# Kernel tuning notes

Measured on AMD Instinct MI355X. Metric: run time of the kernel, lower is better.

Reference implementation:

```python
import jax, jax.numpy as jnp
import numpy as np

B, H, W, ENC = 32, 14, 14, 2048
T = 21            # sequence length; 20 decode steps
V, E, A, L = 10000, 512, 512, 512
P = H * W


def setup_inputs() -> dict:
    key = jax.random.key(0)
    ks = jax.random.split(key, 24)
    g = lambda k, shape, s=0.02: (jax.random.normal(k, shape, jnp.float32) * s)
    return {
        "encoder_output": jax.random.normal(ks[0], (B, H, W, ENC), jnp.float32),
        # tokens in [1, V) so sign/abs length count gives full-length sequences
        "sequences": jax.random.randint(ks[1], (B, T), 1, V).astype(jnp.int64),
        "emb": g(ks[2], (V, E)),
        "Wea": g(ks[3], (ENC, A)), "bea": jnp.zeros((A,), jnp.float32),
        "Wga": g(ks[4], (L, A)),   "bga": jnp.zeros((A,), jnp.float32),
        "Wfa": g(ks[5], (A, 1)),   "bfa": jnp.zeros((1,), jnp.float32),
        "Wl": g(ks[6], (E + ENC, 4 * L)), "Ul": g(ks[7], (L, 4 * L)),
        "bl": jnp.zeros((4 * L,), jnp.float32),
        "Wim": g(ks[8], (ENC, L)), "bim": jnp.zeros((L,), jnp.float32),
        "Wic": g(ks[9], (ENC, L)), "bic": jnp.zeros((L,), jnp.float32),
        "Wb": g(ks[10], (L, ENC)), "bb": jnp.zeros((ENC,), jnp.float32),
        "Wo": g(ks[11], (L, V)),   "bo": jnp.zeros((V,), jnp.float32),
    }


def reference(encoder_output, sequences, emb, Wea, bea, Wga, bga, Wfa, bfa,
              Wl, Ul, bl, Wim, bim, Wic, bic, Wb, bb, Wo, bo):
    # --- sort by descending length (packed-sequence style) ---
    lengths = jnp.sum(jnp.sign(jnp.abs(sequences)), axis=1).astype(jnp.int32)
    order = jnp.argsort(-lengths)
    lengths = lengths[order] - 1                       # number of decode steps per row
    enc = encoder_output[order].reshape(B, P, ENC)     # [B, P, ENC]
    seqs = sequences[order]

    # --- init LSTM states from mean-pooled encoder features ---
    mean = enc.mean(axis=1)                            # [B, ENC]
    h0 = mean @ Wim + bim                              # 'memory_state' (plays role of h)
    c0 = mean @ Wic + bic                              # 'carry_state'  (plays role of c)

    # encoder side of additive attention is time-invariant: hoist out of the loop
    a1 = enc @ Wea + bea                               # [B, P, A]

    steps = T - 1
    toks = seqs[:, :steps].T                           # [steps, B] teacher-forced inputs
    masks = lengths[None, :] > jnp.arange(steps)[:, None]  # [steps, B] active rows

    def step(carry, xs):
        h, c = carry
        tok, m = xs
        # additive attention on carry (cell) state, as in the original code
        a2 = c @ Wga + bga                                         # [B, A]
        e = jnp.squeeze(jax.nn.relu(a1 + a2[:, None, :]) @ Wfa + bfa, -1)  # [B, P]
        alpha = jax.nn.softmax(e, axis=1)
        awe = jnp.einsum('bpe,bp->be', enc, alpha)                 # [B, ENC]
        beta = jax.nn.sigmoid(c @ Wb + bb)                         # gating
        x = jnp.concatenate([emb[tok], awe * beta], axis=1)        # [B, E+ENC]
        # Keras LSTMCell: gate order i, f, g, o
        z = x @ Wl + h @ Ul + bl
        zi, zf, zg, zo = jnp.split(z, 4, axis=1)
        c_new = jax.nn.sigmoid(zf) * c + jax.nn.sigmoid(zi) * jnp.tanh(zg)
        h_new = jax.nn.sigmoid(zo) * jnp.tanh(c_new)
        mf = m[:, None].astype(h.dtype)
        h_new = h_new * mf                 # zero-pad finished rows (packed semantics)
        c_new = c_new * mf
        pred = (c_new @ Wo + bo) * mf      # prediction from carry (cell) state, dropout off
        return (h_new, c_new), (pred, alpha * mf)

    (_, _), (preds, alphas) = jax.lax.scan(step, (h0, c0), (toks, masks))
    return preds.transpose(1, 0, 2), alphas.transpose(1, 0, 2), order
```

## Files before the change

### kernel.cpp

```cpp
#include <hip/hip_runtime.h>
#include <math.h>

#define B_    32
#define T_    21
#define STEPS 20
#define V_    10000
#define E_    512
#define A_    512
#define L_    512
#define P_    196
#define ENC_  2048
#define XW_   3072
#define NT2_  792
#define N2_   12672

#define WS_ORD    0
#define WS_SLEN   32
#define WS_CBUF   64
#define WS_CB     32832
#define WS_XB     41024
#define WS_A2S    90176
#define WS_ESH    106560
#define WS_BETA   114752
#define WS_PZ4    180288
#define WS_A1B    442432
#define WS_WZP    2048064
#define WS_WCP    5193792
#define WS_MEAN   8437824
#define WS_PH     8503360
#define WS_WEAT   9027648

#define OUT_PRED  0
#define OUT_ALPHA 6400000
#define OUT_ORDER 6525440

typedef __attribute__((ext_vector_type(8))) short bf16x8;
typedef __attribute__((ext_vector_type(4))) float f32x4;
typedef unsigned short ushort_t;

__device__ inline unsigned f2bf2(float lo, float hi) {
    unsigned a = __float_as_uint(lo), b = __float_as_uint(hi);
    a = (a + 0x7FFFu + ((a >> 16) & 1u)) >> 16;
    b = (b + 0x7FFFu + ((b >> 16) & 1u)) >> 16;
    return a | (b << 16);
}
__device__ inline ushort_t f2bf(float f) {
    unsigned u = __float_as_uint(f);
    return (ushort_t)((u + 0x7FFFu + ((u >> 16) & 1u)) >> 16);
}
__device__ inline float bfu_lo(unsigned u) { return __uint_as_float(u << 16); }
__device__ inline float bfu_hi(unsigned u) { return __uint_as_float(u & 0xFFFF0000u); }

__global__ void k_order(const int* __restrict__ seqs, int* __restrict__ ord,
                        int* __restrict__ slen, float* __restrict__ out_ord)
{
    __shared__ int len[B_];
    int i = threadIdx.x;
    if (i < B_) {
        int c = 0;
        for (int t = 0; t < T_; ++t) c += (seqs[i * T_ + t] != 0) ? 1 : 0;
        len[i] = c;
    }
    __syncthreads();
    if (i < B_) {
        int li = len[i], r = 0;
        for (int j = 0; j < B_; ++j) {
            int lj = len[j];
            if (lj > li || (lj == li && j < i)) ++r;
        }
        ord[r] = i; slen[r] = li - 1; out_ord[r] = (float)i;
    }
}

__global__ void k_mean(const float* __restrict__ enc, const int* __restrict__ ord,
                       float* __restrict__ mean)
{
    int tid = blockIdx.x * 256 + threadIdx.x;
    int b = tid >> 11, e = tid & 2047;
    const float* row = enc + (size_t)ord[b] * (P_ * ENC_) + e;
    float s = 0.f;
    for (int p = 0; p < P_; ++p) s += row[(size_t)p * ENC_];
    mean[tid] = s * (1.0f / 196.0f);
}

__global__ void k_castWT(const float* __restrict__ Wea, ushort_t* __restrict__ WT)
{
    int tid = blockIdx.x * 256 + threadIdx.x;
    int n = tid >> 11, k = tid & 2047;
    WT[tid] = f2bf(Wea[(size_t)k * 512 + n]);
}

__global__ void sg_partial(const float* __restrict__ X, const float* __restrict__ W,
                           float* __restrict__ part, int K, int N, int kchunk, int chunk_ofs)
{
    const int n = blockIdx.x * 256 + threadIdx.x;
    const int c = blockIdx.y;
    const int bh = blockIdx.z;
    const int k0 = c * kchunk;
    int k1 = k0 + kchunk; if (k1 > K) k1 = K;
    float acc[16];
#pragma unroll
    for (int b = 0; b < 16; ++b) acc[b] = 0.f;
    if (n < N) {
        const float* Xb = X + (size_t)(bh * 16) * K;
        for (int k = k0; k < k1; k += 4) {
            float w0 = W[(size_t)(k + 0) * N + n];
            float w1 = W[(size_t)(k + 1) * N + n];
            float w2 = W[(size_t)(k + 2) * N + n];
            float w3 = W[(size_t)(k + 3) * N + n];
#pragma unroll
            for (int b = 0; b < 16; ++b) {
                const float4 xv = *reinterpret_cast<const float4*>(&Xb[(size_t)b * K + k]);
                acc[b] += xv.x * w0 + xv.y * w1 + xv.z * w2 + xv.w * w3;
            }
        }
        float* po = part + (size_t)(chunk_ofs + c) * (B_ * (size_t)N) + (size_t)(bh * 16) * N;
#pragma unroll
        for (int b = 0; b < 16; ++b) po[(size_t)b * N + n] = acc[b];
    }
}

__global__ void k_h0c0(const float* __restrict__ ph, const float* __restrict__ bim,
                       const float* __restrict__ bic, float* __restrict__ c0,
                       ushort_t* __restrict__ cB, ushort_t* __restrict__ XB)
{
    int tid = blockIdx.x * 256 + threadIdx.x;
    int half = tid >> 14;
    int idx = tid & 16383;
    int l = idx & 511, b = idx >> 9;
    int cofs = half ? 16 : 0;
    float s = 0.f;
    for (int c = 0; c < 16; ++c) s += ph[(size_t)(cofs + c) * (B_ * 512) + idx];
    if (half) {
        float cv = s + bic[l];
        c0[idx] = cv;
        cB[idx] = f2bf(cv);
    } else {
        XB[(size_t)b * XW_ + 2560 + l] = f2bf(s + bim[l]);
    }
}

__global__ __launch_bounds__(256, 1) void k_a1_mfma(
    const float* __restrict__ enc, const ushort_t* __restrict__ WeaT,
    const float* __restrict__ bea, const int* __restrict__ ord,
    ushort_t* __restrict__ a1b)
{
    __shared__ ushort_t As[2][128 * 40];
    __shared__ ushort_t Bs[2][128 * 40];
    const int tid = threadIdx.x;
    const int lane = tid & 63, wave = tid >> 6;
    const int m0 = blockIdx.x * 128;
    const int n0 = blockIdx.y * 128;

    const int c0 = tid, c1 = tid + 256;
    const int ar0 = c0 >> 2, ak0 = (c0 & 3) * 8;
    const int ar1 = c1 >> 2, ak1 = (c1 & 3) * 8;
    const int g0 = m0 + ar0, g1 = m0 + ar1;
    const float* Ag0 = enc + ((size_t)ord[g0 / P_] * P_ + (g0 % P_)) * ENC_ + ak0;
    const float* Ag1 = enc + ((size_t)ord[g1 / P_] * P_ + (g1 % P_)) * ENC_ + ak1;
    const ushort_t* Bg0 = WeaT + (size_t)(n0 + ar0) * ENC_ + ak0;
    const ushort_t* Bg1 = WeaT + (size_t)(n0 + ar1) * ENC_ + ak1;
    const int ao0 = ar0 * 40 + ak0, ao1 = ar1 * 40 + ak1;

    const int wm = (wave >> 1) * 64, wn = (wave & 1) * 64;
    f32x4 acc[4][4] = {};

    {
        float4 v0 = *reinterpret_cast<const float4*>(Ag0);
        float4 v1 = *reinterpret_cast<const float4*>(Ag0 + 4);
        float4 v2 = *reinterpret_cast<const float4*>(Ag1);
        float4 v3 = *reinterpret_cast<const float4*>(Ag1 + 4);
        uint4 pa0, pa1;
        pa0.x = f2bf2(v0.x, v0.y); pa0.y = f2bf2(v0.z, v0.w);
        pa0.z = f2bf2(v1.x, v1.y); pa0.w = f2bf2(v1.z, v1.w);
        pa1.x = f2bf2(v2.x, v2.y); pa1.y = f2bf2(v2.z, v2.w);
        pa1.z = f2bf2(v3.x, v3.y); pa1.w = f2bf2(v3.z, v3.w);
        *reinterpret_cast<uint4*>(&As[0][ao0]) = pa0;
        *reinterpret_cast<uint4*>(&As[0][ao1]) = pa1;
        *reinterpret_cast<uint4*>(&Bs[0][ao0]) = *reinterpret_cast<const uint4*>(Bg0);
        *reinterpret_cast<uint4*>(&Bs[0][ao1]) = *reinterpret_cast<const uint4*>(Bg1);
    }
    __syncthreads();

    for (int it = 0; it < 64; ++it) {
        const int cur = it & 1;
        uint4 npa0, npa1, npb0, npb1;
        const bool more = (it < 63);
        if (more) {
            const int k0 = (it + 1) * 32;
            float4 v0 = *reinterpret_cast<const float4*>(Ag0 + k0);
            float4 v1 = *reinterpret_cast<const float4*>(Ag0 + k0 + 4);
            float4 v2 = *reinterpret_cast<const float4*>(Ag1 + k0);
            float4 v3 = *reinterpret_cast<const float4*>(Ag1 + k0 + 4);
            npa0.x = f2bf2(v0.x, v0.y); npa0.y = f2bf2(v0.z, v0.w);
            npa0.z = f2bf2(v1.x, v1.y); npa0.w = f2bf2(v1.z, v1.w);
            npa1.x = f2bf2(v2.x, v2.y); npa1.y = f2bf2(v2.z, v2.w);
            npa1.z = f2bf2(v3.x, v3.y); npa1.w = f2bf2(v3.z, v3.w);
            npb0 = *reinterpret_cast<const uint4*>(Bg0 + k0);
            npb1 = *reinterpret_cast<const uint4*>(Bg1 + k0);
        }
        {
            bf16x8 af[4], bfr[4];
            const int arow = wm + (lane & 15);
            const int brow = wn + (lane & 15);
            const int koff = (lane >> 4) * 8;
#pragma unroll
            for (int mt = 0; mt < 4; ++mt)
                af[mt] = *reinterpret_cast<const bf16x8*>(&As[cur][(arow + mt * 16) * 40 + koff]);
#pragma unroll
            for (int nt = 0; nt < 4; ++nt)
                bfr[nt] = *reinterpret_cast<const bf16x8*>(&Bs[cur][(brow + nt * 16) * 40 + koff]);
#pragma unroll
            for (int mt = 0; mt < 4; ++mt)
#pragma unroll
                for (int nt = 0; nt < 4; ++nt)
                    acc[mt][nt] = __builtin_amdgcn_mfma_f32_16x16x32_bf16(
                        af[mt], bfr[nt], acc[mt][nt], 0, 0, 0);
        }
        if (more) {
            const int nxt = cur ^ 1;
            *reinterpret_cast<uint4*>(&As[nxt][ao0]) = npa0;
            *reinterpret_cast<uint4*>(&As[nxt][ao1]) = npa1;
            *reinterpret_cast<uint4*>(&Bs[nxt][ao0]) = npb0;
            *reinterpret_cast<uint4*>(&Bs[nxt][ao1]) = npb1;
        }
        __syncthreads();
    }
    const int rbase = (lane >> 4) * 4;
    const int cbase = lane & 15;
#pragma unroll
    for (int nt = 0; nt < 4; ++nt) {
        int col = n0 + wn + nt * 16 + cbase;
        float be = bea[col];
#pragma unroll
        for (int mt = 0; mt < 4; ++mt) {
            int row = m0 + wm + mt * 16 + rbase;
#pragma unroll
            for (int r = 0; r < 4; ++r)
                a1b[(size_t)(row + r) * 512 + col] = f2bf(acc[mt][nt][r] + be);
        }
    }
}

__global__ void k_packWz(const float* __restrict__ Wl, const float* __restrict__ Ul,
                         ushort_t* __restrict__ Wz)
{
    const unsigned tidg = blockIdx.x * 256 + threadIdx.x;
    const int l = tidg & 63;
    const unsigned rem = tidg >> 6;
    const int kt = rem % 96;
    const int nt = rem / 96;
    const int k = kt * 32 + ((l >> 4) << 3);
    const int n = nt * 16 + (l & 15);
    float v[8];
#pragma unroll
    for (int j = 0; j < 8; ++j) {
        int kr = k + j;
        v[j] = (kr < 2560) ? Wl[(size_t)kr * 2048 + n] : Ul[(size_t)(kr - 2560) * 2048 + n];
    }
    uint4 o;
    o.x = f2bf2(v[0], v[1]); o.y = f2bf2(v[2], v[3]);
    o.z = f2bf2(v[4], v[5]); o.w = f2bf2(v[6], v[7]);
    *reinterpret_cast<uint4*>(Wz + (size_t)tidg * 8) = o;
}

__global__ void k_packWc(const float* __restrict__ Wb, const float* __restrict__ Wga,
                         const float* __restrict__ Wo, ushort_t* __restrict__ Wc)
{
    const unsigned tidg = blockIdx.x * 256 + threadIdx.x;
    const int l = tidg & 63;
    const int kt = (tidg >> 6) & 15;
    const int nt = tidg >> 10;
    const int k = kt * 32 + ((l >> 4) << 3);
    const int n = nt * 16 + (l & 15);
    float v[8];
#pragma unroll
    for (int j = 0; j < 8; ++j) {
        int kr = k + j;
        float x;
        if (n < 2048)            x = Wb[(size_t)kr * 2048 + n];
        else if (n < 2560)       x = Wga[(size_t)kr * 512 + (n - 2048)];
        else if (n < 2560 + V_)  x = Wo[(size_t)kr * V_ + (n - 2560)];
        else                     x = 0.f;
        v[j] = x;
    }
    uint4 o;
    o.x = f2bf2(v[0], v[1]); o.y = f2bf2(v[2], v[3]);
    o.z = f2bf2(v[4], v[5]); o.w = f2bf2(v[6], v[7]);
    *reinterpret_cast<uint4*>(Wc + (size_t)tidg * 8) = o;
}

__global__ __launch_bounds__(256, 1) void k_e(
    const float* __restrict__ a2s, const float* __restrict__ Wfa,
    const float* __restrict__ bfa, const ushort_t* __restrict__ a1b,
    float* __restrict__ eshW)
{
    __shared__ float a2sh[512];
    __shared__ float wfsh[512];
    const int b = blockIdx.x >> 2, pc = blockIdx.x & 3;
    const int tid = threadIdx.x;
    const int wave = tid >> 6, lane = tid & 63;
    a2sh[tid] = a2s[b * 512 + tid];       a2sh[tid + 256] = a2s[b * 512 + 256 + tid];
    wfsh[tid] = Wfa[tid];                 wfsh[tid + 256] = Wfa[256 + tid];
    __syncthreads();

    const int grp = lane >> 4, sub = lane & 15;
    float4 a2r[4][2], wfr[4][2];
#pragma unroll
    for (int blk = 0; blk < 4; ++blk)
#pragma unroll
        for (int j = 0; j < 2; ++j) {
            int d = blk * 128 + sub * 8 + j * 4;
            a2r[blk][j] = *reinterpret_cast<const float4*>(&a2sh[d]);
            wfr[blk][j] = *reinterpret_cast<const float4*>(&wfsh[d]);
        }
    const float bf0 = bfa[0];
    const int p0 = pc * 49;
#pragma unroll
    for (int pass = 0; pass < 4; ++pass) {
        const int pl = pass * 16 + wave * 4 + grp;
        const bool valid = pl < 49;
        const int p = p0 + (valid ? pl : 0);
        const ushort_t* arow = a1b + ((size_t)b * P_ + p) * 512;
        float s = 0.f;
#pragma unroll
        for (int blk = 0; blk < 4; ++blk) {
            uint4 raw = *reinterpret_cast<const uint4*>(arow + blk * 128 + sub * 8);
            float4 av = a2r[blk][0], wv = wfr[blk][0];
            float v;
            v = bfu_lo(raw.x) + av.x; v = v > 0.f ? v : 0.f; s += v * wv.x;
            v = bfu_hi(raw.x) + av.y; v = v > 0.f ? v : 0.f; s += v * wv.y;
            v = bfu_lo(raw.y) + av.z; v = v > 0.f ? v : 0.f; s += v * wv.z;
            v = bfu_hi(raw.y) + av.w; v = v > 0.f ? v : 0.f; s += v * wv.w;
            av = a2r[blk][1]; wv = wfr[blk][1];
            v = bfu_lo(raw.z) + av.x; v = v > 0.f ? v : 0.f; s += v * wv.x;
            v = bfu_hi(raw.z) + av.y; v = v > 0.f ? v : 0.f; s += v * wv.y;
            v = bfu_lo(raw.w) + av.z; v = v > 0.f ? v : 0.f; s += v * wv.z;
            v = bfu_hi(raw.w) + av.w; v = v > 0.f ? v : 0.f; s += v * wv.w;
        }
        s += __shfl_xor(s, 1, 64);
        s += __shfl_xor(s, 2, 64);
        s += __shfl_xor(s, 4, 64);
        s += __shfl_xor(s, 8, 64);
        if (sub == 0 && valid) eshW[b * 256 + p0 + pl] = s + bf0;
    }
}

__global__ __launch_bounds__(256, 1) void k_awex(
    const float* __restrict__ eshW, const float* __restrict__ enc,
    const int* __restrict__ ord, const int* __restrict__ slen, int t,
    const float* __restrict__ beta, float* __restrict__ out_alpha,
    ushort_t* __restrict__ XB)
{
    __shared__ float red[256];
    __shared__ float alsh[P_];
    const int b = blockIdx.x >> 2, ec = blockIdx.x & 3;
    const int tid = threadIdx.x;

    float v = (tid < P_) ? eshW[b * 256 + tid] : -1e30f;
    red[tid] = v; __syncthreads();
    for (int s2 = 128; s2 > 0; s2 >>= 1) {
        if (tid < s2) red[tid] = fmaxf(red[tid], red[tid + s2]);
        __syncthreads();
    }
    float mx = red[0]; __syncthreads();
    float ex = (tid < P_) ? expf(v - mx) : 0.f;
    red[tid] = ex; __syncthreads();
    for (int s2 = 128; s2 > 0; s2 >>= 1) {
        if (tid < s2) red[tid] += red[tid + s2];
        __syncthreads();
    }
    float inv = 1.0f / red[0];
    float al = ex * inv;
    if (tid < P_) alsh[tid] = al;
    if (ec == 0 && tid < P_) {
        float mf = (slen[b] > t) ? 1.f : 0.f;
        out_alpha[((size_t)b * STEPS + t) * P_ + tid] = al * mf;
    }
    __syncthreads();

    const int e0 = ec * 512 + tid * 2;
    const float* ep = enc + (size_t)ord[b] * (P_ * ENC_) + e0;
    float s0 = 0.f, s1 = 0.f;
    for (int p = 0; p < P_; ++p) {
        float2 u = *reinterpret_cast<const float2*>(ep + (size_t)p * ENC_);
        float ap = alsh[p];
        s0 += ap * u.x; s1 += ap * u.y;
    }
    float2 bt = *reinterpret_cast<const float2*>(&beta[b * 2048 + e0]);
    unsigned pk = f2bf2(s0 * bt.x, s1 * bt.y);
    *reinterpret_cast<unsigned*>(XB + (size_t)b * XW_ + 512 + e0) = pk;
}

__global__ __launch_bounds__(256) void k_zmfma(const ushort_t* __restrict__ XB,
                                               const ushort_t* __restrict__ WzP,
                                               float* __restrict__ pz4)
{
    const int tid = threadIdx.x, lane = tid & 63, w = tid >> 6;
    const int nt = blockIdx.x * 4 + w;
    const int kt0 = blockIdx.y * 24;
    const int ar = lane & 15, ak = (lane >> 4) * 8;
    const ushort_t* A0 = XB + (size_t)ar * XW_ + kt0 * 32 + ak;
    const ushort_t* Bp = WzP + ((size_t)nt * 96 + kt0) * 512 + lane * 8;
    f32x4 acc0 = {}, acc1 = {};
    for (int kt = 0; kt < 24; ++kt) {
        bf16x8 a0 = *reinterpret_cast<const bf16x8*>(A0 + kt * 32);
        bf16x8 a1 = *reinterpret_cast<const bf16x8*>(A0 + 16 * XW_ + kt * 32);
        bf16x8 bf = *reinterpret_cast<const bf16x8*>(Bp + kt * 512);
        acc0 = __builtin_amdgcn_mfma_f32_16x16x32_bf16(a0, bf, acc0, 0, 0, 0);
        acc1 = __builtin_amdgcn_mfma_f32_16x16x32_bf16(a1, bf, acc1, 0, 0, 0);
    }
    const int col = nt * 16 + (lane & 15);
    const int r0 = (lane >> 4) * 4;
    float* po = pz4 + (size_t)blockIdx.y * 65536 + col;
#pragma unroll
    for (int r = 0; r < 4; ++r) {
        po[(size_t)(r0 + r) * 2048] = acc0[r];
        po[(size_t)(16 + r0 + r) * 2048] = acc1[r];
    }
}

__global__ void k_gates(const float* __restrict__ pz4, const float* __restrict__ bl,
                        const float* __restrict__ c_in, const int* __restrict__ slen, int t,
                        float* __restrict__ c_out, ushort_t* __restrict__ cB,
                        ushort_t* __restrict__ XB)
{
    int tid = blockIdx.x * 256 + threadIdx.x;
    int b = tid >> 9, l = tid & 511;
    float zi = 0.f, zf = 0.f, zg = 0.f, zo = 0.f;
#pragma unroll
    for (int kc = 0; kc < 4; ++kc) {
        const float* row = pz4 + (size_t)kc * 65536 + b * 2048;
        zi += row[l]; zf += row[512 + l]; zg += row[1024 + l]; zo += row[1536 + l];
    }
    zi += bl[l]; zf += bl[512 + l]; zg += bl[1024 + l]; zo += bl[1536 + l];
    float si = 1.f / (1.f + expf(-zi));
    float sf = 1.f / (1.f + expf(-zf));
    float so = 1.f / (1.f + expf(-zo));
    float g  = tanhf(zg);
    float cn = sf * c_in[tid] + si * g;
    float hn = so * tanhf(cn);
    float mf = (slen[b] > t) ? 1.f : 0.f;
    cn *= mf; hn *= mf;
    c_out[tid] = cn;
    cB[tid] = f2bf(cn);
    XB[(size_t)b * XW_ + 2560 + l] = f2bf(hn);
}

__global__ __launch_bounds__(256) void k_cmfma(
    const ushort_t* __restrict__ cB, const ushort_t* __restrict__ WcP,
    const float* __restrict__ bb, const float* __restrict__ bga, const float* __restrict__ bo,
    const int* __restrict__ slen, int t, int do_pred, int tnext,
    const int* __restrict__ seqs, const float* __restrict__ emb, const int* __restrict__ ord,
    float* __restrict__ beta, float* __restrict__ a2s, float* __restrict__ out_pred,
    ushort_t* __restrict__ XB)
{
    const int bid = blockIdx.x, tid = threadIdx.x;
    if (bid >= 99) {
        const int g = (bid - 99) * 256 + tid;
        const int b = g >> 4, j0 = (g & 15) * 32;
        const int tok = seqs[ord[b] * T_ + tnext];
        const float4* src = reinterpret_cast<const float4*>(emb + (size_t)tok * E_ + j0);
        uint4* dst = reinterpret_cast<uint4*>(XB + (size_t)b * XW_ + j0);
#pragma unroll
        for (int q = 0; q < 4; ++q) {
            float4 v0 = src[2 * q], v1 = src[2 * q + 1];
            uint4 o;
            o.x = f2bf2(v0.x, v0.y); o.y = f2bf2(v0.z, v0.w);
            o.z = f2bf2(v1.x, v1.y); o.w = f2bf2(v1.z, v1.w);
            dst[q] = o;
        }
        return;
    }
    const int lane = tid & 63, w = tid >> 6;
    const int nt0 = bid * 8 + w * 2;
    const int ar = lane & 15, ak = (lane >> 4) * 8;
    const ushort_t* A0 = cB + ar * 512 + ak;
    const ushort_t* Bp = WcP + (size_t)nt0 * 8192 + lane * 8;
    f32x4 acc[2][2] = {};
    for (int kt = 0; kt < 16; ++kt) {
        bf16x8 a0 = *reinterpret_cast<const bf16x8*>(A0 + kt * 32);
        bf16x8 a1 = *reinterpret_cast<const bf16x8*>(A0 + 16 * 512 + kt * 32);
        bf16x8 b0 = *reinterpret_cast<const bf16x8*>(Bp + kt * 512);
        bf16x8 b1 = *reinterpret_cast<const bf16x8*>(Bp + 8192 + kt * 512);
        acc[0][0] = __builtin_amdgcn_mfma_f32_16x16x32_bf16(a0, b0, acc[0][0], 0, 0, 0);
        acc[0][1] = __builtin_amdgcn_mfma_f32_16x16x32_bf16(a0, b1, acc[0][1], 0, 0, 0);
        acc[1][0] = __builtin_amdgcn_mfma_f32_16x16x32_bf16(a1, b0, acc[1][0], 0, 0, 0);
        acc[1][1] = __builtin_amdgcn_mfma_f32_16x16x32_bf16(a1, b1, acc[1][1], 0, 0, 0);
    }
    const int r0 = (lane >> 4) * 4, cb = lane & 15;
#pragma unroll
    for (int nti = 0; nti < 2; ++nti) {
        const int n = (nt0 + nti) * 16 + cb;
#pragma unroll
        for (int mt = 0; mt < 2; ++mt) {
#pragma unroll
            for (int r = 0; r < 4; ++r) {
                const int brow = mt * 16 + r0 + r;
                float v = acc[mt][nti][r];
                if (n < 2048) {
                    beta[brow * 2048 + n] = 1.f / (1.f + expf(-(v + bb[n])));
                } else if (n < 2560) {
                    a2s[brow * 512 + (n - 2048)] = v + bga[n - 2048];
                } else if (n < 2560 + V_) {
                    if (do_pred) {
                        float mf = (slen[brow] > t) ? 1.f : 0.f;
                        out_pred[((size_t)brow * STEPS + t) * V_ + (n - 2560)] =
                            (v + bo[n - 2560]) * mf;
                    }
                }
            }
        }
    }
}

extern "C" void kernel_launch(void* const* d_in, const int* in_sizes, int n_in,
                              void* d_out, int out_size, void* d_ws, size_t ws_size,
                              hipStream_t stream)
{
    const float* enc  = (const float*)d_in[0];
    const int*   seqs = (const int*)  d_in[1];
    const float* emb  = (const float*)d_in[2];
    const float* Wea  = (const float*)d_in[3];
    const float* bea  = (const float*)d_in[4];
    const float* Wga  = (const float*)d_in[5];
    const float* bga  = (const float*)d_in[6];
    const float* Wfa  = (const float*)d_in[7];
    const float* bfa  = (const float*)d_in[8];
    const float* Wl   = (const float*)d_in[9];
    const float* Ul   = (const float*)d_in[10];
    const float* bl   = (const float*)d_in[11];
    const float* Wim  = (const float*)d_in[12];
    const float* bim  = (const float*)d_in[13];
    const float* Wic  = (const float*)d_in[14];
    const float* bic  = (const float*)d_in[15];
    const float* Wb   = (const float*)d_in[16];
    const float* bb   = (const float*)d_in[17];
    const float* Wo   = (const float*)d_in[18];
    const float* bo   = (const float*)d_in[19];

    float* out = (float*)d_out;
    float* ws  = (float*)d_ws;
    int* ord  = (int*)(ws + WS_ORD);
    int* slen = (int*)(ws + WS_SLEN);
    ushort_t* cBu  = (ushort_t*)(ws + WS_CB);
    ushort_t* XB   = (ushort_t*)(ws + WS_XB);
    ushort_t* a1b  = (ushort_t*)(ws + WS_A1B);
    ushort_t* WzP  = (ushort_t*)(ws + WS_WZP);
    ushort_t* WcP  = (ushort_t*)(ws + WS_WCP);
    ushort_t* WeaT = (ushort_t*)(ws + WS_WEAT);
    float* a2s  = ws + WS_A2S;
    float* eshW = ws + WS_ESH;
    float* beta = ws + WS_BETA;
    float* pz4  = ws + WS_PZ4;

    k_order<<<1, 64, 0, stream>>>(seqs, ord, slen, out + OUT_ORDER);
    k_mean<<<256, 256, 0, stream>>>(enc, ord, ws + WS_MEAN);
    sg_partial<<<dim3(2, 16, 2), 256, 0, stream>>>(ws + WS_MEAN, Wim, ws + WS_PH, 2048, 512, 128, 0);
    sg_partial<<<dim3(2, 16, 2), 256, 0, stream>>>(ws + WS_MEAN, Wic, ws + WS_PH, 2048, 512, 128, 16);
    k_h0c0<<<128, 256, 0, stream>>>(ws + WS_PH, bim, bic, ws + WS_CBUF, cBu, XB);
    k_castWT<<<4096, 256, 0, stream>>>(Wea, WeaT);
    k_a1_mfma<<<dim3(49, 4), 256, 0, stream>>>(enc, WeaT, bea, ord, a1b);
    k_packWz<<<3072, 256, 0, stream>>>(Wl, Ul, WzP);
    k_packWc<<<3168, 256, 0, stream>>>(Wb, Wga, Wo, WcP);
    k_cmfma<<<101, 256, 0, stream>>>(cBu, WcP, bb, bga, bo, slen, 0, 0, 0,
                                     seqs, emb, ord, beta, a2s, out + OUT_PRED, XB);

    for (int t = 0; t < STEPS; ++t) {
        float* c_in  = ws + WS_CBUF + (t & 1) * (B_ * L_);
        float* c_out = ws + WS_CBUF + ((t + 1) & 1) * (B_ * L_);

        k_e<<<128, 256, 0, stream>>>(a2s, Wfa, bfa, a1b, eshW);
        k_awex<<<128, 256, 0, stream>>>(eshW, enc, ord, slen, t, beta, out + OUT_ALPHA, XB);
        k_zmfma<<<dim3(32, 4), 256, 0, stream>>>(XB, WzP, pz4);
        k_gates<<<64, 256, 0, stream>>>(pz4, bl, c_in, slen, t, c_out, cBu, XB);
        k_cmfma<<<101, 256, 0, stream>>>(cBu, WcP, bb, bga, bo, slen, t, 1, t + 1,
                                         seqs, emb, ord, beta, a2s, out + OUT_PRED, XB);
    }
}
```

Before: 1.132 ms.

## Batch output projection across all steps and fuse attention score with weighted sum

The vocabulary projection (c @ Wo) is taken out of the recurrent loop. Each step's bf16 cell state is stored into a per-step buffer, and one large MFMA GEMM (640 x 10000 x 512) runs after the loop, so Wo is streamed once instead of twenty times. The per-step kernel now only computes the beta and a2 columns, which shrinks it to 22 blocks. The attention-score kernel and the softmax/weighted-sum kernel are fused into one kernel that keeps scores in shared memory and splits the pixel range across waves. Workspace regions for the setup-only buffers are aliased onto the packed weight areas to make room for the per-step cell states.

```diff
diff --git a/kernel.cpp b/kernel.cpp
--- a/kernel.cpp
+++ b/kernel.cpp
@@ -11,24 +11,22 @@
 #define P_    196
 #define ENC_  2048
 #define XW_   3072
-#define NT2_  792
-#define N2_   12672
 
 #define WS_ORD    0
 #define WS_SLEN   32
 #define WS_CBUF   64
-#define WS_CB     32832
-#define WS_XB     41024
-#define WS_A2S    90176
-#define WS_ESH    106560
-#define WS_BETA   114752
-#define WS_PZ4    180288
-#define WS_A1B    442432
-#define WS_WZP    2048064
-#define WS_WCP    5193792
-#define WS_MEAN   8437824
-#define WS_PH     8503360
-#define WS_WEAT   9027648
+#define WS_CB0    32832
+#define WS_CBALL  36928
+#define WS_XB     200768
+#define WS_A2S    249920
+#define WS_BETA   266304
+#define WS_PZ4    331840
+#define WS_A1B    593984
+#define WS_WZP    2199616
+#define WS_WCP    5345344
+#define WS_MEAN   (WS_WZP)
+#define WS_PH     (WS_WZP + 65536)
+#define WS_WEAT   (WS_WCP)
 
 #define OUT_PRED  0
 #define OUT_ALPHA 6400000
@@ -122,7 +120,7 @@
 
 __global__ void k_h0c0(const float* __restrict__ ph, const float* __restrict__ bim,
                        const float* __restrict__ bic, float* __restrict__ c0,
-                       ushort_t* __restrict__ cB, ushort_t* __restrict__ XB)
+                       ushort_t* __restrict__ cB0, ushort_t* __restrict__ XB)
 {
     int tid = blockIdx.x * 256 + threadIdx.x;
     int half = tid >> 14;
@@ -134,7 +132,7 @@
     if (half) {
         float cv = s + bic[l];
         c0[idx] = cv;
-        cB[idx] = f2bf(cv);
+        cB0[idx] = f2bf(cv);
     } else {
         XB[(size_t)b * XW_ + 2560 + l] = f2bf(s + bim[l]);
     }
@@ -290,14 +288,19 @@
     *reinterpret_cast<uint4*>(Wc + (size_t)tidg * 8) = o;
 }
 
-__global__ __launch_bounds__(256, 1) void k_e(
+__global__ __launch_bounds__(256, 1) void k_eawex(
     const float* __restrict__ a2s, const float* __restrict__ Wfa,
     const float* __restrict__ bfa, const ushort_t* __restrict__ a1b,
-    float* __restrict__ eshW)
+    const float* __restrict__ enc, const int* __restrict__ ord,
+    const int* __restrict__ slen, int t, const float* __restrict__ beta,
+    float* __restrict__ out_alpha, ushort_t* __restrict__ XB)
 {
     __shared__ float a2sh[512];
     __shared__ float wfsh[512];
-    const int b = blockIdx.x >> 2, pc = blockIdx.x & 3;
+    __shared__ float esh[208];
+    __shared__ float red[256];
+    __shared__ float part[4][512];
+    const int b = blockIdx.x >> 2, ec = blockIdx.x & 3;
     const int tid = threadIdx.x;
     const int wave = tid >> 6, lane = tid & 63;
     a2sh[tid] = a2s[b * 512 + tid];       a2sh[tid + 256] = a2s[b * 512 + 256 + tid];
@@ -315,12 +318,11 @@
             wfr[blk][j] = *reinterpret_cast<const float4*>(&wfsh[d]);
         }
     const float bf0 = bfa[0];
-    const int p0 = pc * 49;
-#pragma unroll
-    for (int pass = 0; pass < 4; ++pass) {
+#pragma unroll
+    for (int pass = 0; pass < 13; ++pass) {
         const int pl = pass * 16 + wave * 4 + grp;
-        const bool valid = pl < 49;
-        const int p = p0 + (valid ? pl : 0);
+        const bool valid = pl < P_;
+        const int p = valid ? pl : 0;
         const ushort_t* arow = a1b + ((size_t)b * P_ + p) * 512;
         float s = 0.f;
 #pragma unroll
@@ -342,22 +344,11 @@
         s += __shfl_xor(s, 2, 64);
         s += __shfl_xor(s, 4, 64);
         s += __shfl_xor(s, 8, 64);
-        if (sub == 0 && valid) eshW[b * 256 + p0 + pl] = s + bf0;
-    }
-}
-
-__global__ __launch_bounds__(256, 1) void k_awex(
-    const float* __restrict__ eshW, const float* __restrict__ enc,
-    const int* __restrict__ ord, const int* __restrict__ slen, int t,
-    const float* __restrict__ beta, float* __restrict__ out_alpha,
-    ushort_t* __restrict__ XB)
-{
-    __shared__ float red[256];
-    __shared__ float alsh[P_];
-    const int b = blockIdx.x >> 2, ec = blockIdx.x & 3;
-    const int tid = threadIdx.x;
-
-    float v = (tid < P_) ? eshW[b * 256 + tid] : -1e30f;
+        if (sub == 0 && valid) esh[pl] = s + bf0;
+    }
+    __syncthreads();
+
+    float v = (tid < P_) ? esh[tid] : -1e30f;
     red[tid] = v; __syncthreads();
     for (int s2 = 128; s2 > 0; s2 >>= 1) {
         if (tid < s2) red[tid] = fmaxf(red[tid], red[tid + s2]);
@@ -372,24 +363,34 @@
     }
     float inv = 1.0f / red[0];
     float al = ex * inv;
-    if (tid < P_) alsh[tid] = al;
+    __syncthreads();
+    if (tid < P_) esh[tid] = al;
     if (ec == 0 && tid < P_) {
         float mf = (slen[b] > t) ? 1.f : 0.f;
         out_alpha[((size_t)b * STEPS + t) * P_ + tid] = al * mf;
     }
     __syncthreads();
 
-    const int e0 = ec * 512 + tid * 2;
-    const float* ep = enc + (size_t)ord[b] * (P_ * ENC_) + e0;
-    float s0 = 0.f, s1 = 0.f;
-    for (int p = 0; p < P_; ++p) {
-        float2 u = *reinterpret_cast<const float2*>(ep + (size_t)p * ENC_);
-        float ap = alsh[p];
-        s0 += ap * u.x; s1 += ap * u.y;
-    }
-    float2 bt = *reinterpret_cast<const float2*>(&beta[b * 2048 + e0]);
-    unsigned pk = f2bf2(s0 * bt.x, s1 * bt.y);
-    *reinterpret_cast<unsigned*>(XB + (size_t)b * XW_ + 512 + e0) = pk;
+    const int col0 = ec * 512 + lane * 8;
+    const float* ep = enc + (size_t)ord[b] * (P_ * ENC_) + (size_t)wave * 49 * ENC_ + col0;
+    float s8[8] = {0.f, 0.f, 0.f, 0.f, 0.f, 0.f, 0.f, 0.f};
+    for (int i = 0; i < 49; ++i) {
+        float ap = esh[wave * 49 + i];
+        float4 u0 = *reinterpret_cast<const float4*>(ep + (size_t)i * ENC_);
+        float4 u1 = *reinterpret_cast<const float4*>(ep + (size_t)i * ENC_ + 4);
+        s8[0] += ap * u0.x; s8[1] += ap * u0.y; s8[2] += ap * u0.z; s8[3] += ap * u0.w;
+        s8[4] += ap * u1.x; s8[5] += ap * u1.y; s8[6] += ap * u1.z; s8[7] += ap * u1.w;
+    }
+#pragma unroll
+    for (int j = 0; j < 8; ++j) part[wave][lane * 8 + j] = s8[j];
+    __syncthreads();
+    const int cc = tid * 2;
+    float r0 = part[0][cc] + part[1][cc] + part[2][cc] + part[3][cc];
+    float r1 = part[0][cc + 1] + part[1][cc + 1] + part[2][cc + 1] + part[3][cc + 1];
+    const int col = ec * 512 + cc;
+    float2 bt = *reinterpret_cast<const float2*>(&beta[b * 2048 + col]);
+    unsigned pk = f2bf2(r0 * bt.x, r1 * bt.y);
+    *reinterpret_cast<unsigned*>(XB + (size_t)b * XW_ + 512 + col) = pk;
 }
 
 __global__ __launch_bounds__(256) void k_zmfma(const ushort_t* __restrict__ XB,
@@ -422,7 +423,7 @@
 
 __global__ void k_gates(const float* __restrict__ pz4, const float* __restrict__ bl,
                         const float* __restrict__ c_in, const int* __restrict__ slen, int t,
-                        float* __restrict__ c_out, ushort_t* __restrict__ cB,
+                        float* __restrict__ c_out, ushort_t* __restrict__ cB_slot,
                         ushort_t* __restrict__ XB)
 {
     int tid = blockIdx.x * 256 + threadIdx.x;
@@ -443,21 +444,20 @@
     float mf = (slen[b] > t) ? 1.f : 0.f;
     cn *= mf; hn *= mf;
     c_out[tid] = cn;
-    cB[tid] = f2bf(cn);
+    cB_slot[tid] = f2bf(cn);
     XB[(size_t)b * XW_ + 2560 + l] = f2bf(hn);
 }
 
-__global__ __launch_bounds__(256) void k_cmfma(
+__global__ __launch_bounds__(256) void k_cmfma_lite(
     const ushort_t* __restrict__ cB, const ushort_t* __restrict__ WcP,
-    const float* __restrict__ bb, const float* __restrict__ bga, const float* __restrict__ bo,
-    const int* __restrict__ slen, int t, int do_pred, int tnext,
-    const int* __restrict__ seqs, const float* __restrict__ emb, const int* __restrict__ ord,
-    float* __restrict__ beta, float* __restrict__ a2s, float* __restrict__ out_pred,
-    ushort_t* __restrict__ XB)
+    const float* __restrict__ bb, const float* __restrict__ bga,
+    int tnext, const int* __restrict__ seqs, const float* __restrict__ emb,
+    const int* __restrict__ ord,
+    float* __restrict__ beta, float* __restrict__ a2s, ushort_t* __restrict__ XB)
 {
     const int bid = blockIdx.x, tid = threadIdx.x;
-    if (bid >= 99) {
-        const int g = (bid - 99) * 256 + tid;
+    if (bid >= 20) {
+        const int g = (bid - 20) * 256 + tid;
         const int b = g >> 4, j0 = (g & 15) * 32;
         const int tok = seqs[ord[b] * T_ + tnext];
         const float4* src = reinterpret_cast<const float4*>(emb + (size_t)tok * E_ + j0);
@@ -500,14 +500,58 @@
                 float v = acc[mt][nti][r];
                 if (n < 2048) {
                     beta[brow * 2048 + n] = 1.f / (1.f + expf(-(v + bb[n])));
-                } else if (n < 2560) {
+                } else {
                     a2s[brow * 512 + (n - 2048)] = v + bga[n - 2048];
-                } else if (n < 2560 + V_) {
-                    if (do_pred) {
-                        float mf = (slen[brow] > t) ? 1.f : 0.f;
-                        out_pred[((size_t)brow * STEPS + t) * V_ + (n - 2560)] =
-                            (v + bo[n - 2560]) * mf;
-                    }
+                }
+            }
+        }
+    }
+}
+
+__global__ __launch_bounds__(256) void k_pred(
+    const ushort_t* __restrict__ cBall, const ushort_t* __restrict__ WcP,
+    const float* __restrict__ bo, const int* __restrict__ slen,
+    float* __restrict__ out_pred)
+{
+    const int tid = threadIdx.x, lane = tid & 63, w = tid >> 6;
+    const int n0 = blockIdx.x * 128;
+    const int m0 = blockIdx.y * 128;
+    const int wm = (w >> 1) * 64, wn = (w & 1) * 64;
+    const int ar = lane & 15, ak = (lane >> 4) * 8;
+    const int ntb = (2560 + n0 + wn) >> 4;
+    f32x4 acc[4][4] = {};
+    for (int kt = 0; kt < 16; ++kt) {
+        bf16x8 af[4], bfr[4];
+#pragma unroll
+        for (int mt = 0; mt < 4; ++mt)
+            af[mt] = *reinterpret_cast<const bf16x8*>(
+                cBall + (size_t)(m0 + wm + mt * 16 + ar) * 512 + kt * 32 + ak);
+#pragma unroll
+        for (int nt = 0; nt < 4; ++nt)
+            bfr[nt] = *reinterpret_cast<const bf16x8*>(
+                WcP + ((size_t)(ntb + nt) * 16 + kt) * 512 + lane * 8);
+#pragma unroll
+        for (int mt = 0; mt < 4; ++mt)
+#pragma unroll
+            for (int nt = 0; nt < 4; ++nt)
+                acc[mt][nt] = __builtin_amdgcn_mfma_f32_16x16x32_bf16(
+                    af[mt], bfr[nt], acc[mt][nt], 0, 0, 0);
+    }
+    const int r0 = (lane >> 4) * 4, cb = lane & 15;
+#pragma unroll
+    for (int nt = 0; nt < 4; ++nt) {
+        const int n = n0 + wn + nt * 16 + cb;
+        if (n < V_) {
+            const float bv = bo[n];
+#pragma unroll
+            for (int mt = 0; mt < 4; ++mt) {
+#pragma unroll
+                for (int r = 0; r < 4; ++r) {
+                    const int m = m0 + wm + mt * 16 + r0 + r;
+                    const int tt = m >> 5, bb_ = m & 31;
+                    const float mf = (slen[bb_] > tt) ? 1.f : 0.f;
+                    out_pred[((size_t)bb_ * STEPS + tt) * V_ + n] =
+                        (acc[mt][nt][r] + bv) * mf;
                 }
             }
         }
@@ -543,14 +587,14 @@
     float* ws  = (float*)d_ws;
     int* ord  = (int*)(ws + WS_ORD);
     int* slen = (int*)(ws + WS_SLEN);
-    ushort_t* cBu  = (ushort_t*)(ws + WS_CB);
-    ushort_t* XB   = (ushort_t*)(ws + WS_XB);
-    ushort_t* a1b  = (ushort_t*)(ws + WS_A1B);
-    ushort_t* WzP  = (ushort_t*)(ws + WS_WZP);
-    ushort_t* WcP  = (ushort_t*)(ws + WS_WCP);
-    ushort_t* WeaT = (ushort_t*)(ws + WS_WEAT);
+    ushort_t* cB0   = (ushort_t*)(ws + WS_CB0);
+    ushort_t* cBall = (ushort_t*)(ws + WS_CBALL);
+    ushort_t* XB    = (ushort_t*)(ws + WS_XB);
+    ushort_t* a1b   = (ushort_t*)(ws + WS_A1B);
+    ushort_t* WzP   = (ushort_t*)(ws + WS_WZP);
+    ushort_t* WcP   = (ushort_t*)(ws + WS_WCP);
+    ushort_t* WeaT  = (ushort_t*)(ws + WS_WEAT);
     float* a2s  = ws + WS_A2S;
-    float* eshW = ws + WS_ESH;
     float* beta = ws + WS_BETA;
     float* pz4  = ws + WS_PZ4;
 
@@ -558,23 +602,25 @@
     k_mean<<<256, 256, 0, stream>>>(enc, ord, ws + WS_MEAN);
     sg_partial<<<dim3(2, 16, 2), 256, 0, stream>>>(ws + WS_MEAN, Wim, ws + WS_PH, 2048, 512, 128, 0);
     sg_partial<<<dim3(2, 16, 2), 256, 0, stream>>>(ws + WS_MEAN, Wic, ws + WS_PH, 2048, 512, 128, 16);
-    k_h0c0<<<128, 256, 0, stream>>>(ws + WS_PH, bim, bic, ws + WS_CBUF, cBu, XB);
+    k_h0c0<<<128, 256, 0, stream>>>(ws + WS_PH, bim, bic, ws + WS_CBUF, cB0, XB);
     k_castWT<<<4096, 256, 0, stream>>>(Wea, WeaT);
     k_a1_mfma<<<dim3(49, 4), 256, 0, stream>>>(enc, WeaT, bea, ord, a1b);
     k_packWz<<<3072, 256, 0, stream>>>(Wl, Ul, WzP);
     k_packWc<<<3168, 256, 0, stream>>>(Wb, Wga, Wo, WcP);
-    k_cmfma<<<101, 256, 0, stream>>>(cBu, WcP, bb, bga, bo, slen, 0, 0, 0,
-                                     seqs, emb, ord, beta, a2s, out + OUT_PRED, XB);
+    k_cmfma_lite<<<22, 256, 0, stream>>>(cB0, WcP, bb, bga, 0, seqs, emb, ord,
+                                         beta, a2s, XB);
 
     for (int t = 0; t < STEPS; ++t) {
         float* c_in  = ws + WS_CBUF + (t & 1) * (B_ * L_);
         float* c_out = ws + WS_CBUF + ((t + 1) & 1) * (B_ * L_);
-
-        k_e<<<128, 256, 0, stream>>>(a2s, Wfa, bfa, a1b, eshW);
-        k_awex<<<128, 256, 0, stream>>>(eshW, enc, ord, slen, t, beta, out + OUT_ALPHA, XB);
+        ushort_t* cB_slot = cBall + (size_t)t * (B_ * L_);
+
+        k_eawex<<<128, 256, 0, stream>>>(a2s, Wfa, bfa, a1b, enc, ord, slen, t,
+                                         beta, out + OUT_ALPHA, XB);
         k_zmfma<<<dim3(32, 4), 256, 0, stream>>>(XB, WzP, pz4);
-        k_gates<<<64, 256, 0, stream>>>(pz4, bl, c_in, slen, t, c_out, cBu, XB);
-        k_cmfma<<<101, 256, 0, stream>>>(cBu, WcP, bb, bga, bo, slen, t, 1, t + 1,
-                                         seqs, emb, ord, beta, a2s, out + OUT_PRED, XB);
-    }
-}
+        k_gates<<<64, 256, 0, stream>>>(pz4, bl, c_in, slen, t, c_out, cB_slot, XB);
+        k_cmfma_lite<<<22, 256, 0, stream>>>(cB_slot, WcP, bb, bga, t + 1, seqs, emb, ord,
+                                             beta, a2s, XB);
+    }
+    k_pred<<<dim3(79, 5), 256, 0, stream>>>(cBall, WcP, bo, slen, out + OUT_PRED);
+}
```

Result: slower. 1.230 ms (+8.7%).
